# Kernel optimization log

Measured on AMD Instinct MI355X. Metric: run time of the kernel, lower is better.

Reference implementation:

```python
import jax, jax.numpy as jnp
import numpy as np

K = 3  # de_neighbors
NUM_STAGES = 4


def _square_distance(a, b):
    # a: [B,N,3], b: [B,S,3] -> [B,N,S] squared euclidean distances
    return (jnp.sum(a * a, -1)[:, :, None]
            + jnp.sum(b * b, -1)[:, None, :]
            - 2.0 * jnp.einsum('bnd,bsd->bns', a, b))


def _propagate(xyz1, xyz2, points1, points2, k):
    # xyz1: [B,N,3] fine coords; xyz2: [B,S,3] coarse coords
    # points1: [B,C1,N] skip feats (or None); points2: [B,C2,S] coarse feats
    p2 = jnp.transpose(points2, (0, 2, 1))  # [B,S,C2]
    N = xyz1.shape[1]
    S = xyz2.shape[1]
    if S == 1:
        interp = jnp.tile(p2, (1, N, 1))
    else:
        d = _square_distance(xyz1, xyz2)            # [B,N,S]
        neg_d, idx = jax.lax.top_k(-d, k)           # k smallest dists
        dk = -neg_d                                 # [B,N,k]
        w = 1.0 / (dk + 1e-8)
        w = w / jnp.sum(w, axis=-1, keepdims=True)  # [B,N,k]
        gathered = jax.vmap(lambda p, i: p[i])(p2, idx)  # [B,N,k,C2]
        interp = jnp.sum(gathered * w[..., None], axis=2)  # [B,N,C2]
    if points1 is not None:
        interp = jnp.concatenate([jnp.transpose(points1, (0, 2, 1)), interp], axis=-1)
    return jnp.transpose(interp, (0, 2, 1))  # [B,C1+C2,N]


def setup_inputs() -> dict:
    key = jax.random.key(0)
    ks = jax.random.split(key, 10)
    B = 16
    Ns = [4096, 1024, 256, 64, 16]
    Cs = [64, 128, 256, 512, 1024]
    out = {}
    for i in range(5):
        out[f'xyz{i}'] = jax.random.normal(ks[i], (B, Ns[i], 3), dtype=jnp.float32)
        out[f'f{i}'] = jax.random.normal(ks[5 + i], (B, Cs[i], Ns[i]), dtype=jnp.float32)
    return out


def reference(xyz0, xyz1, xyz2, xyz3, xyz4, f0, f1, f2, f3, f4):
    # forward() reverses the fine->coarse lists to coarse->fine
    xyz = [xyz4, xyz3, xyz2, xyz1, xyz0]
    feats = [f4, f3, f2, f1, f0]
    x = feats[0]
    for i in range(NUM_STAGES):
        x = _propagate(xyz[i + 1], xyz[i], feats[i + 1], x, K)
    return x  # [B, 1984, 4096]
```

## Files before the change

kernel.cpp:

```cpp
#include <hip/hip_runtime.h>

#define B 16
typedef float f32x4 __attribute__((ext_vector_type(4)));

__global__ __launch_bounds__(256) void knn_all_kernel(
    const float* __restrict__ xyz0, const float* __restrict__ xyz1,
    const float* __restrict__ xyz2, const float* __restrict__ xyz3,
    const float* __restrict__ xyz4, const float* __restrict__ f0,
    float* __restrict__ out,
    int4* idx0, float4* w0, int4* idx1, float4* w1,
    int4* idx2, float4* w2, int4* idx3, float4* w3) {
    __shared__ float lds[(256 + 1) * 4 * 4];
    int bid = blockIdx.x;
    if (bid >= 1360) {
        bid -= 1360;
        const int b = bid >> 3;
        const int c0 = (bid & 7) * 8;
        const f32x4* src = reinterpret_cast<const f32x4*>(f0 + ((size_t)b * 64 + c0) * 4096);
        f32x4* dst = reinterpret_cast<f32x4*>(out + ((size_t)b * 1984 + c0) * 4096);
        for (int i = threadIdx.x; i < 8 * 1024; i += 256) {
            __builtin_nontemporal_store(__builtin_nontemporal_load(src + i), dst + i);
        }
        return;
    }
    int S, logS4;
    const float *xf, *xc;
    int4* io; float4* wo;
    if (bid < 1024)      { S = 1024; logS4 = 8; xf = xyz0; xc = xyz1; io = idx3; wo = w3; }
    else if (bid < 1280) { bid -= 1024; S = 256; logS4 = 6; xf = xyz1; xc = xyz2; io = idx2; wo = w2; }
    else if (bid < 1344) { bid -= 1280; S = 64;  logS4 = 4; xf = xyz2; xc = xyz3; io = idx1; wo = w1; }
    else                 { bid -= 1344; S = 16;  logS4 = 2; xf = xyz3; xc = xyz4; io = idx0; wo = w0; }
    const int N = S << 2;
    const int lognb = logS4 - 2;
    const int b = bid >> lognb;
    const int nblk = bid & ((1 << lognb) - 1);
    const int S4 = S >> 2;

    const float* cbase = xc + (size_t)b * S * 3;
    for (int j = threadIdx.x; j < S; j += 256) {
        float x = cbase[j * 3 + 0], y = cbase[j * 3 + 1], z = cbase[j * 3 + 2];
        int seg = j >> logS4, jj = j & (S4 - 1);
        float* p = lds + (size_t)(seg * (S4 + 1) + jj) * 4;
        p[0] = x; p[1] = y; p[2] = z; p[3] = x * x + y * y + z * z;
    }
    __syncthreads();
    const int t = threadIdx.x;
    const int sub = t & 3;
    const int n = nblk * 64 + (t >> 2);
    const float* fp = xf + ((size_t)b * N + n) * 3;
    const float ax = fp[0], ay = fp[1], az = fp[2];
    const float an2 = ax * ax + ay * ay + az * az;
    float d0 = 1e30f, d1 = 1e30f, d2 = 1e30f;
    int i0 = -1, i1 = -1, i2 = -1;
    const f32x4* seg4 = reinterpret_cast<const f32x4*>(lds) + sub * (S4 + 1);
    const int jbase = sub * S4;
#pragma unroll 4
    for (int k = 0; k < S4; ++k) {
        f32x4 c = seg4[k];
        float d = an2 + c[3] - 2.0f * (ax * c[0] + ay * c[1] + az * c[2]);
        int j = jbase + k;
        if (d < d2) {
            if (d < d1) {
                d2 = d1; i2 = i1;
                if (d < d0) { d1 = d0; i1 = i0; d0 = d; i0 = j; }
                else        { d1 = d;  i1 = j; }
            } else { d2 = d; i2 = j; }
        }
    }
#pragma unroll
    for (int r = 1; r <= 2; r <<= 1) {
        float e0 = __shfl_xor(d0, r), e1 = __shfl_xor(d1, r), e2 = __shfl_xor(d2, r);
        int   j0 = __shfl_xor(i0, r), j1 = __shfl_xor(i1, r), j2 = __shfl_xor(i2, r);
        float ed[3] = {e0, e1, e2};
        int   ej[3] = {j0, j1, j2};
#pragma unroll
        for (int m = 0; m < 3; ++m) {
            float d = ed[m]; int j = ej[m];
            if (d < d0 || (d == d0 && j < i0)) {
                d2 = d1; i2 = i1; d1 = d0; i1 = i0; d0 = d; i0 = j;
            } else if (d < d1 || (d == d1 && j < i1)) {
                d2 = d1; i2 = i1; d1 = d; i1 = j;
            } else if (d < d2 || (d == d2 && j < i2)) {
                d2 = d; i2 = j;
            }
        }
    }
    if (sub == 0) {
        float w0_ = 1.0f / (d0 + 1e-8f);
        float w1_ = 1.0f / (d1 + 1e-8f);
        float w2_ = 1.0f / (d2 + 1e-8f);
        float inv = 1.0f / (w0_ + w1_ + w2_);
        size_t o = (size_t)b * N + n;
        io[o] = make_int4(i0, i1, i2, 0);
        wo[o] = make_float4(w0_ * inv, w1_ * inv, w2_ * inv, 0.0f);
    }
}


template <int P>
__device__ __forceinline__ void copy_planes(const float* __restrict__ src_rows,
                                            f32x4* dst, int t) {
    constexpr int P4 = P / 4;
    const f32x4* src = reinterpret_cast<const f32x4*>(src_rows);
    float* df = reinterpret_cast<float*>(dst);
    for (int e = t; e < 8 * P4; e += 256) {
        int c = e / P4;
        int s4 = e & (P4 - 1);
        f32x4 v = src[c * P4 + s4];
        int base = (((c >> 2) * P + s4 * 4) << 2) + (c & 3);
        df[base + 0] = v[0]; df[base + 4] = v[1];
        df[base + 8] = v[2]; df[base + 12] = v[3];
    }
}

template <int PD, int PS>
__device__ __forceinline__ void expand(const f32x4* src, f32x4* dst,
                                       const int4* __restrict__ idxL,
                                       const f32x4* __restrict__ wL,
                                       int b, int t) {
    for (int e = t; e < 2 * PD; e += 256) {
        int p = (e >= PD) ? 1 : 0;
        int s = e - p * PD;
        int4 id = idxL[(size_t)b * PD + s];
        f32x4 ww = wL[(size_t)b * PD + s];
        const f32x4* sp = src + p * PS;
        dst[e] = ww[0] * sp[id.x] + ww[1] * sp[id.y] + ww[2] * sp[id.z];
    }
}

__global__ __launch_bounds__(256) void decode_kernel(
    const float* __restrict__ f1, const float* __restrict__ f2,
    const float* __restrict__ f3, const float* __restrict__ f4,
    const int4* __restrict__ idx0, const f32x4* __restrict__ w0,
    const int4* __restrict__ idx1, const f32x4* __restrict__ w1,
    const int4* __restrict__ idx2, const f32x4* __restrict__ w2,
    const int4* __restrict__ idx3, const f32x4* __restrict__ w3,
    float* __restrict__ out) {
    __shared__ f32x4 buf[2560];
    f32x4* s3 = buf;
    f32x4* s2 = buf + 2048;
    f32x4* s1 = buf;
    f32x4* s0 = buf + 128;
    const int b = blockIdx.x;
    const int cx = (239 - blockIdx.y) * 8;
    const int t = threadIdx.x;
    float* outb = out + ((size_t)b * 1984 + 64 + cx) * 4096;

    if (cx < 128) {
        copy_planes<1024>(f1 + ((size_t)b * 128 + cx) * 1024, s3, t);
        __syncthreads();
    } else if (cx < 384) {
        copy_planes<256>(f2 + ((size_t)b * 256 + (cx - 128)) * 256, s2, t);
        __syncthreads();
        expand<1024, 256>(s2, s3, idx2, w2, b, t);
        __syncthreads();
    } else if (cx < 896) {
        copy_planes<64>(f3 + ((size_t)b * 512 + (cx - 384)) * 64, s1, t);
        __syncthreads();
        expand<256, 64>(s1, s2, idx1, w1, b, t);
        __syncthreads();
        expand<1024, 256>(s2, s3, idx2, w2, b, t);
        __syncthreads();
    } else {
        copy_planes<16>(f4 + ((size_t)b * 1024 + (cx - 896)) * 16, s0, t);
        __syncthreads();
        expand<64, 16>(s0, s1, idx0, w0, b, t);
        __syncthreads();
        expand<256, 64>(s1, s2, idx1, w1, b, t);
        __syncthreads();
        expand<1024, 256>(s2, s3, idx2, w2, b, t);
        __syncthreads();
    }
    const int4* idxF = idx3 + (size_t)b * 4096;
    const f32x4* wF = w3 + (size_t)b * 4096;
#pragma unroll 2
    for (int it = 0; it < 4; ++it) {
        const int n0 = (it * 256 + t) * 4;
        int4 id[4]; f32x4 ww[4];
#pragma unroll
        for (int q = 0; q < 4; ++q) { id[q] = idxF[n0 + q]; ww[q] = wF[n0 + q]; }
#pragma unroll
        for (int p = 0; p < 2; ++p) {
            const f32x4* pl = s3 + p * 1024;
            f32x4 v[4];
#pragma unroll
            for (int q = 0; q < 4; ++q) {
                v[q] = ww[q][0] * pl[id[q].x] + ww[q][1] * pl[id[q].y]
                     + ww[q][2] * pl[id[q].z];
            }
            float* ob = outb + (size_t)(p * 4) * 4096 + n0;
#pragma unroll
            for (int j = 0; j < 4; ++j) {
                f32x4 st = {v[0][j], v[1][j], v[2][j], v[3][j]};
                __builtin_nontemporal_store(st, reinterpret_cast<f32x4*>(ob + (size_t)j * 4096));
            }
        }
    }
}

extern "C" void kernel_launch(void* const* d_in, const int* in_sizes, int n_in,
                              void* d_out, int out_size, void* d_ws, size_t ws_size,
                              hipStream_t stream) {
    static const int xyzSz[5] = {16 * 4096 * 3, 16 * 1024 * 3, 16 * 256 * 3,
                                 16 * 64 * 3, 16 * 16 * 3};
    static const int fSz[5] = {16 * 64 * 4096, 16 * 128 * 1024, 16 * 256 * 256,
                               16 * 512 * 64, 16 * 1024 * 16};
    const float* xyz[5] = {nullptr, nullptr, nullptr, nullptr, nullptr};
    const float* f[5] = {nullptr, nullptr, nullptr, nullptr, nullptr};
    for (int i = 0; i < n_in; ++i) {
        for (int j = 0; j < 5; ++j) {
            if (in_sizes[i] == xyzSz[j] && !xyz[j]) { xyz[j] = (const float*)d_in[i]; goto next; }
            if (in_sizes[i] == fSz[j] && !f[j])     { f[j] = (const float*)d_in[i];  goto next; }
        }
    next:;
    }

    char* ws = (char*)d_ws;
    int4*   idx3 = (int4*)(ws);
    float4* w3   = (float4*)(ws + (1u << 20));
    int4*   idx2 = (int4*)(ws + (2u << 20));
    float4* w2   = (float4*)(ws + (2u << 20) + 262144u);
    int4*   idx1 = (int4*)(ws + (2u << 20) + 524288u);
    float4* w1   = (float4*)(ws + (2u << 20) + 589824u);
    int4*   idx0 = (int4*)(ws + (2u << 20) + 655360u);
    float4* w0   = (float4*)(ws + (2u << 20) + 671744u);

    knn_all_kernel<<<1488, 256, 0, stream>>>(
        xyz[0], xyz[1], xyz[2], xyz[3], xyz[4], f[0], (float*)d_out,
        idx0, w0, idx1, w1, idx2, w2, idx3, w3);

    decode_kernel<<<dim3(B, 240), 256, 0, stream>>>(
        f[1], f[2], f[3], f[4],
        idx0, (const f32x4*)w0, idx1, (const f32x4*)w1,
        idx2, (const f32x4*)w2, idx3, (const f32x4*)w3,
        (float*)d_out);
}
```

Measured before the change: 130.4 us.

## Pack kNN indices and weights into one float4 and halve decode channel tile

```diff
diff --git a/kernel.cpp b/kernel.cpp
--- a/kernel.cpp
+++ b/kernel.cpp
@@ -2,14 +2,18 @@
 
 #define B 16
 typedef float f32x4 __attribute__((ext_vector_type(4)));
+
+__device__ __forceinline__ void unpack_pw(const f32x4 pw, int& i0, int& i1, int& i2) {
+    unsigned p = __float_as_uint(pw[0]);
+    i0 = p & 1023; i1 = (p >> 10) & 1023; i2 = p >> 20;
+}
 
 __global__ __launch_bounds__(256) void knn_all_kernel(
     const float* __restrict__ xyz0, const float* __restrict__ xyz1,
     const float* __restrict__ xyz2, const float* __restrict__ xyz3,
     const float* __restrict__ xyz4, const float* __restrict__ f0,
     float* __restrict__ out,
-    int4* idx0, float4* w0, int4* idx1, float4* w1,
-    int4* idx2, float4* w2, int4* idx3, float4* w3) {
+    f32x4* pw0, f32x4* pw1, f32x4* pw2, f32x4* pw3) {
     __shared__ float lds[(256 + 1) * 4 * 4];
     int bid = blockIdx.x;
     if (bid >= 1360) {
@@ -25,11 +29,11 @@
     }
     int S, logS4;
     const float *xf, *xc;
-    int4* io; float4* wo;
-    if (bid < 1024)      { S = 1024; logS4 = 8; xf = xyz0; xc = xyz1; io = idx3; wo = w3; }
-    else if (bid < 1280) { bid -= 1024; S = 256; logS4 = 6; xf = xyz1; xc = xyz2; io = idx2; wo = w2; }
-    else if (bid < 1344) { bid -= 1280; S = 64;  logS4 = 4; xf = xyz2; xc = xyz3; io = idx1; wo = w1; }
-    else                 { bid -= 1344; S = 16;  logS4 = 2; xf = xyz3; xc = xyz4; io = idx0; wo = w0; }
+    f32x4* po;
+    if (bid < 1024)      { S = 1024; logS4 = 8; xf = xyz0; xc = xyz1; po = pw3; }
+    else if (bid < 1280) { bid -= 1024; S = 256; logS4 = 6; xf = xyz1; xc = xyz2; po = pw2; }
+    else if (bid < 1344) { bid -= 1280; S = 64;  logS4 = 4; xf = xyz2; xc = xyz3; po = pw1; }
+    else                 { bid -= 1344; S = 16;  logS4 = 2; xf = xyz3; xc = xyz4; po = pw0; }
     const int N = S << 2;
     const int lognb = logS4 - 2;
     const int b = bid >> lognb;
@@ -90,24 +94,24 @@
         float w1_ = 1.0f / (d1 + 1e-8f);
         float w2_ = 1.0f / (d2 + 1e-8f);
         float inv = 1.0f / (w0_ + w1_ + w2_);
-        size_t o = (size_t)b * N + n;
-        io[o] = make_int4(i0, i1, i2, 0);
-        wo[o] = make_float4(w0_ * inv, w1_ * inv, w2_ * inv, 0.0f);
+        unsigned packed = (unsigned)i0 | ((unsigned)i1 << 10) | ((unsigned)i2 << 20);
+        f32x4 pw = {__uint_as_float(packed), w0_ * inv, w1_ * inv, w2_ * inv};
+        po[(size_t)b * N + n] = pw;
     }
 }
 
 
 template <int P>
-__device__ __forceinline__ void copy_planes(const float* __restrict__ src_rows,
-                                            f32x4* dst, int t) {
+__device__ __forceinline__ void copy_plane(const float* __restrict__ src_rows,
+                                           f32x4* dst, int t) {
     constexpr int P4 = P / 4;
     const f32x4* src = reinterpret_cast<const f32x4*>(src_rows);
     float* df = reinterpret_cast<float*>(dst);
-    for (int e = t; e < 8 * P4; e += 256) {
+    for (int e = t; e < 4 * P4; e += 256) {
         int c = e / P4;
         int s4 = e & (P4 - 1);
         f32x4 v = src[c * P4 + s4];
-        int base = (((c >> 2) * P + s4 * 4) << 2) + (c & 3);
+        int base = ((s4 * 4) << 2) + c;
         df[base + 0] = v[0]; df[base + 4] = v[1];
         df[base + 8] = v[2]; df[base + 12] = v[3];
     }
@@ -115,85 +119,71 @@
 
 template <int PD, int PS>
 __device__ __forceinline__ void expand(const f32x4* src, f32x4* dst,
-                                       const int4* __restrict__ idxL,
-                                       const f32x4* __restrict__ wL,
+                                       const f32x4* __restrict__ pwL,
                                        int b, int t) {
-    for (int e = t; e < 2 * PD; e += 256) {
-        int p = (e >= PD) ? 1 : 0;
-        int s = e - p * PD;
-        int4 id = idxL[(size_t)b * PD + s];
-        f32x4 ww = wL[(size_t)b * PD + s];
-        const f32x4* sp = src + p * PS;
-        dst[e] = ww[0] * sp[id.x] + ww[1] * sp[id.y] + ww[2] * sp[id.z];
-    }
-}
-
-__global__ __launch_bounds__(256) void decode_kernel(
+    for (int s = t; s < PD; s += 256) {
+        f32x4 pw = pwL[(size_t)b * PD + s];
+        int i0, i1, i2; unpack_pw(pw, i0, i1, i2);
+        dst[s] = pw[1] * src[i0] + pw[2] * src[i1] + pw[3] * src[i2];
+    }
+}
+
+__global__ __launch_bounds__(256, 8) void decode_kernel(
     const float* __restrict__ f1, const float* __restrict__ f2,
     const float* __restrict__ f3, const float* __restrict__ f4,
-    const int4* __restrict__ idx0, const f32x4* __restrict__ w0,
-    const int4* __restrict__ idx1, const f32x4* __restrict__ w1,
-    const int4* __restrict__ idx2, const f32x4* __restrict__ w2,
-    const int4* __restrict__ idx3, const f32x4* __restrict__ w3,
+    const f32x4* __restrict__ pw0, const f32x4* __restrict__ pw1,
+    const f32x4* __restrict__ pw2, const f32x4* __restrict__ pw3,
     float* __restrict__ out) {
-    __shared__ f32x4 buf[2560];
+    __shared__ f32x4 buf[1280];
     f32x4* s3 = buf;
-    f32x4* s2 = buf + 2048;
+    f32x4* s2 = buf + 1024;
     f32x4* s1 = buf;
-    f32x4* s0 = buf + 128;
+    f32x4* s0 = buf + 64;
     const int b = blockIdx.x;
-    const int cx = (239 - blockIdx.y) * 8;
+    const int cx = (479 - blockIdx.y) * 4;
     const int t = threadIdx.x;
     float* outb = out + ((size_t)b * 1984 + 64 + cx) * 4096;
 
     if (cx < 128) {
-        copy_planes<1024>(f1 + ((size_t)b * 128 + cx) * 1024, s3, t);
+        copy_plane<1024>(f1 + ((size_t)b * 128 + cx) * 1024, s3, t);
         __syncthreads();
     } else if (cx < 384) {
-        copy_planes<256>(f2 + ((size_t)b * 256 + (cx - 128)) * 256, s2, t);
-        __syncthreads();
-        expand<1024, 256>(s2, s3, idx2, w2, b, t);
+        copy_plane<256>(f2 + ((size_t)b * 256 + (cx - 128)) * 256, s2, t);
+        __syncthreads();
+        expand<1024, 256>(s2, s3, pw2, b, t);
         __syncthreads();
     } else if (cx < 896) {
-        copy_planes<64>(f3 + ((size_t)b * 512 + (cx - 384)) * 64, s1, t);
-        __syncthreads();
-        expand<256, 64>(s1, s2, idx1, w1, b, t);
-        __syncthreads();
-        expand<1024, 256>(s2, s3, idx2, w2, b, t);
+        copy_plane<64>(f3 + ((size_t)b * 512 + (cx - 384)) * 64, s1, t);
+        __syncthreads();
+        expand<256, 64>(s1, s2, pw1, b, t);
+        __syncthreads();
+        expand<1024, 256>(s2, s3, pw2, b, t);
         __syncthreads();
     } else {
-        copy_planes<16>(f4 + ((size_t)b * 1024 + (cx - 896)) * 16, s0, t);
-        __syncthreads();
-        expand<64, 16>(s0, s1, idx0, w0, b, t);
-        __syncthreads();
-        expand<256, 64>(s1, s2, idx1, w1, b, t);
-        __syncthreads();
-        expand<1024, 256>(s2, s3, idx2, w2, b, t);
-        __syncthreads();
-    }
-    const int4* idxF = idx3 + (size_t)b * 4096;
-    const f32x4* wF = w3 + (size_t)b * 4096;
+        copy_plane<16>(f4 + ((size_t)b * 1024 + (cx - 896)) * 16, s0, t);
+        __syncthreads();
+        expand<64, 16>(s0, s1, pw0, b, t);
+        __syncthreads();
+        expand<256, 64>(s1, s2, pw1, b, t);
+        __syncthreads();
+        expand<1024, 256>(s2, s3, pw2, b, t);
+        __syncthreads();
+    }
+    const f32x4* pwF = pw3 + (size_t)b * 4096;
 #pragma unroll 2
     for (int it = 0; it < 4; ++it) {
         const int n0 = (it * 256 + t) * 4;
-        int4 id[4]; f32x4 ww[4];
-#pragma unroll
-        for (int q = 0; q < 4; ++q) { id[q] = idxF[n0 + q]; ww[q] = wF[n0 + q]; }
-#pragma unroll
-        for (int p = 0; p < 2; ++p) {
-            const f32x4* pl = s3 + p * 1024;
-            f32x4 v[4];
-#pragma unroll
-            for (int q = 0; q < 4; ++q) {
-                v[q] = ww[q][0] * pl[id[q].x] + ww[q][1] * pl[id[q].y]
-                     + ww[q][2] * pl[id[q].z];
-            }
-            float* ob = outb + (size_t)(p * 4) * 4096 + n0;
-#pragma unroll
-            for (int j = 0; j < 4; ++j) {
-                f32x4 st = {v[0][j], v[1][j], v[2][j], v[3][j]};
-                __builtin_nontemporal_store(st, reinterpret_cast<f32x4*>(ob + (size_t)j * 4096));
-            }
+        f32x4 v[4];
+#pragma unroll
+        for (int q = 0; q < 4; ++q) {
+            f32x4 pw = pwF[n0 + q];
+            int i0, i1, i2; unpack_pw(pw, i0, i1, i2);
+            v[q] = pw[1] * s3[i0] + pw[2] * s3[i1] + pw[3] * s3[i2];
+        }
+#pragma unroll
+        for (int j = 0; j < 4; ++j) {
+            f32x4 st = {v[0][j], v[1][j], v[2][j], v[3][j]};
+            __builtin_nontemporal_store(st, reinterpret_cast<f32x4*>(outb + (size_t)j * 4096 + n0));
         }
     }
 }
@@ -216,22 +206,15 @@
     }
 
     char* ws = (char*)d_ws;
-    int4*   idx3 = (int4*)(ws);
-    float4* w3   = (float4*)(ws + (1u << 20));
-    int4*   idx2 = (int4*)(ws + (2u << 20));
-    float4* w2   = (float4*)(ws + (2u << 20) + 262144u);
-    int4*   idx1 = (int4*)(ws + (2u << 20) + 524288u);
-    float4* w1   = (float4*)(ws + (2u << 20) + 589824u);
-    int4*   idx0 = (int4*)(ws + (2u << 20) + 655360u);
-    float4* w0   = (float4*)(ws + (2u << 20) + 671744u);
+    f32x4* pw3 = (f32x4*)(ws);
+    f32x4* pw2 = (f32x4*)(ws + (1u << 20));
+    f32x4* pw1 = (f32x4*)(ws + (1u << 20) + 262144u);
+    f32x4* pw0 = (f32x4*)(ws + (1u << 20) + 327680u);
 
     knn_all_kernel<<<1488, 256, 0, stream>>>(
         xyz[0], xyz[1], xyz[2], xyz[3], xyz[4], f[0], (float*)d_out,
-        idx0, w0, idx1, w1, idx2, w2, idx3, w3);
-
-    decode_kernel<<<dim3(B, 240), 256, 0, stream>>>(
-        f[1], f[2], f[3], f[4],
-        idx0, (const f32x4*)w0, idx1, (const f32x4*)w1,
-        idx2, (const f32x4*)w2, idx3, (const f32x4*)w3,
-        (float*)d_out);
-}
+        pw0, pw1, pw2, pw3);
+
+    decode_kernel<<<dim3(B, 480), 256, 0, stream>>>(
+        f[1], f[2], f[3], f[4], pw0, pw1, pw2, pw3, (float*)d_out);
+}
```

After: 135.2 us. 1.04x slower.
